# Performance work log

Measured on AMD Instinct MI355X. Metric: run time of the kernel, lower is better.

The kernel has to match this reference:

```python
import jax, jax.numpy as jnp
import numpy as np

D_MODEL = 1024
N_STATE = 64
BASEWIDTH = 3
BC_SCALE = (D_MODEL / BASEWIDTH) ** -0.5  # 'mup' mode width_mult**-0.5
RMS_EPS = 1.1920928955078125e-07  # torch.finfo(float32).eps (RMSNorm eps=None default)


def setup_inputs() -> dict:
    key = jax.random.key(0)
    k1, k2, k3, k4 = jax.random.split(key, 4)
    Bsz, L = 4, 2048
    u = jax.random.normal(k1, (Bsz, D_MODEL, L), dtype=jnp.float32)
    A = jax.random.uniform(k2, (N_STATE,), dtype=jnp.float32) * 0.1  # buffer: rand(N)*A_scale
    B = (jax.random.normal(k3, (N_STATE, D_MODEL), dtype=jnp.float32) + 0.1) * BC_SCALE
    C = (jax.random.normal(k4, (N_STATE, D_MODEL), dtype=jnp.float32) + 0.1) * BC_SCALE
    D = jnp.ones((D_MODEL,), dtype=jnp.float32)
    norm_w = jnp.ones((D_MODEL,), dtype=jnp.float32)
    return {"L": L, "u": u, "A": A, "B": B, "C": C, "D": D, "norm_w": norm_w}


def _ssm(u, A, B, C, D, norm_w):
    # u: [b, d, l]
    scale = BC_SCALE  # applied to Bu, Cu in 'mup' hyperparam mode
    Bu = jnp.einsum('nd,bdl->bnl', B, u) * scale  # [b, n, l]
    Cu = jnp.einsum('nd,bdl->bnl', C, u) * scale  # [b, n, l]
    b, d, l = u.shape
    # shifted_delta == 1 (delta path commented out in source), so
    # h_{t} = A * h_{t-1} + Bu[:, :, t] (outer) u[:, :, t]
    h0 = jnp.zeros((b, d, A.shape[0]), dtype=u.dtype)

    def step(h, xs):
        bu_t, cu_t, u_t = xs  # [b,n], [b,n], [b,d]
        h = h * A + u_t[:, :, None] * bu_t[:, None, :]  # [b, d, n]
        y_t = jnp.einsum('bn,bdn->bd', cu_t, h)
        return h, y_t

    xs = (jnp.moveaxis(Bu, 2, 0), jnp.moveaxis(Cu, 2, 0), jnp.moveaxis(u, 2, 0))
    _, y = jax.lax.scan(step, h0, xs)  # y: [l, b, d]
    y = jnp.moveaxis(y, 0, 2).transpose(1, 0, 2) if False else jnp.transpose(y, (1, 2, 0))  # [b, d, l]
    out = y + u * D[None, :, None]
    # RMSNorm over d_model (apply in [b, l, d] layout)
    x = jnp.transpose(out, (0, 2, 1))  # [b, l, d]
    ms = jnp.mean(x * x, axis=-1, keepdims=True)
    x = x * jax.lax.rsqrt(ms + RMS_EPS) * norm_w
    return jnp.transpose(x, (0, 2, 1))  # [b, d, l]


def reference(L, u, A, B, C, D, norm_w):
    del L  # sequence length == u.shape[-1]
    return _ssm(u, A, B, C, D, norm_w)
```

## Files before the change

kernel.cpp:

```cpp
#include <hip/hip_runtime.h>
#include <stdint.h>

#define DM 1024
#define LS 2048
#define RMS_EPS 1.1920928955078125e-07f
#define S2 0.0029296875f

typedef __attribute__((ext_vector_type(8))) short bf16x8;
typedef __attribute__((ext_vector_type(4))) float f32x4;
typedef __attribute__((ext_vector_type(2))) unsigned int u32x2;

__device__ __forceinline__ unsigned short f2bf(float f) {
  uint32_t u = __builtin_bit_cast(uint32_t, f);
  u += 0x7FFFu + ((u >> 16) & 1u);
  return (unsigned short)(u >> 16);
}

__global__ __launch_bounds__(256) void k0_prep(const float* __restrict__ B,
                                               const float* __restrict__ C,
                                               unsigned short* __restrict__ Bbf) {
  int i4 = blockIdx.x * 256 + threadIdx.x;
  const float4* src = (i4 < 16384) ? (const float4*)B : (const float4*)C;
  float4 v = src[i4 & 16383];
  ushort4 o;
  o.x = f2bf(v.x); o.y = f2bf(v.y); o.z = f2bf(v.z); o.w = f2bf(v.w);
  ((ushort4*)Bbf)[i4] = o;
}

__global__ __launch_bounds__(256) void kg(const float* __restrict__ u,
                                          const unsigned short* __restrict__ Bbf,
                                          const float* __restrict__ A,
                                          float* __restrict__ Kwg) {
  const int wg = blockIdx.x;
  const int sw = (wg & 7) * 64 + (wg >> 3);
  const int b  = sw >> 7;
  const int t0 = (sw & 127) * 16;
  const int tid  = threadIdx.x;
  const int lane = tid & 63;
  const int w    = tid >> 6;
  const int nn = lane & 15, q = lane >> 4;
  const float* ub = u + (size_t)b * DM * LS;

  __shared__ __align__(16) bf16x8 At[2][128][9];
  __shared__ __align__(16) bf16x8 Ut[2][8][33];
  __shared__ float KwS[16][20];
  float (*BuCu)[132] = (float (*)[132])&At[0][0][0];

  bf16x8 areg[4];
  float4 ureg[4];
  const int ukq = tid >> 3;
  const int ulq = tid & 7;
  const int ugc = t0 - 16 + 4*ulq;

  auto LOAD = [&](int kk) {
    #pragma unroll
    for (int h = 0; h < 4; ++h) {
      int id = tid + 256*h;
      areg[h] = *(const bf16x8*)(Bbf + (size_t)(id >> 3) * DM + 64*kk + 8*(id & 7));
    }
    if (tid < 128) {
      if (ugc >= 0) {
        #pragma unroll
        for (int r = 0; r < 4; ++r)
          ureg[r] = *(const float4*)(ub + (size_t)(64*kk + 4*ukq + r) * LS + ugc);
      } else {
        #pragma unroll
        for (int r = 0; r < 4; ++r) ureg[r] = make_float4(0.f, 0.f, 0.f, 0.f);
      }
    }
  };
  auto WRITE = [&](int buf) {
    #pragma unroll
    for (int h = 0; h < 4; ++h) {
      int id = tid + 256*h;
      At[buf][id >> 3][id & 7] = areg[h];
    }
    if (tid < 128) {
      #pragma unroll
      for (int i = 0; i < 4; ++i) {
        u32x2 pk;
        pk[0] = (unsigned)f2bf(((const float*)&ureg[0])[i]) |
                ((unsigned)f2bf(((const float*)&ureg[1])[i]) << 16);
        pk[1] = (unsigned)f2bf(((const float*)&ureg[2])[i]) |
                ((unsigned)f2bf(((const float*)&ureg[3])[i]) << 16);
        char* dst = (char*)&Ut[buf][ukq >> 1][4*ulq + i] + (ukq & 1) * 8;
        *(u32x2*)dst = pk;
      }
    }
  };

  f32x4 acc[2][2] = {};
  auto COMPUTE = [&](int buf) {
    #pragma unroll
    for (int kc = 0; kc < 2; ++kc) {
      bf16x8 bf0 = Ut[buf][4*kc + q][nn];
      bf16x8 bf1 = Ut[buf][4*kc + q][16 + nn];
      #pragma unroll
      for (int rt = 0; rt < 2; ++rt) {
        bf16x8 af = At[buf][32*w + 16*rt + nn][4*kc + q];
        acc[rt][0] = __builtin_amdgcn_mfma_f32_16x16x32_bf16(af, bf0, acc[rt][0], 0, 0, 0);
        acc[rt][1] = __builtin_amdgcn_mfma_f32_16x16x32_bf16(af, bf1, acc[rt][1], 0, 0, 0);
      }
    }
  };

  LOAD(0); WRITE(0); __syncthreads();
  for (int kk = 0; kk < 16; ++kk) {
    if (kk < 15) LOAD(kk + 1);
    COMPUTE(kk & 1);
    __syncthreads();
    if (kk < 15) { WRITE((kk + 1) & 1); __syncthreads(); }
  }

  #pragma unroll
  for (int rt = 0; rt < 2; ++rt)
    #pragma unroll
    for (int cn = 0; cn < 2; ++cn)
      *(f32x4*)&BuCu[16*cn + nn][32*w + 16*rt + 4*q] = acc[rt][cn];
  __syncthreads();

  {
    const int t = tid >> 4, p = tid & 15;
    const float4 cu = *(const float4*)&BuCu[16 + t][64 + 4*p];
    const float4 aa = *(const float4*)(A + 4*p);
    float pw0 = cu.x * S2, pw1 = cu.y * S2, pw2 = cu.z * S2, pw3 = cu.w * S2;
    #pragma unroll
    for (int j = 0; j < 16; ++j) {
      const float4 b4 = *(const float4*)&BuCu[16 + t - j][4*p];
      float s = pw0*b4.x + pw1*b4.y + pw2*b4.z + pw3*b4.w;
      s += __shfl_xor(s, 1, 64);
      s += __shfl_xor(s, 2, 64);
      s += __shfl_xor(s, 4, 64);
      s += __shfl_xor(s, 8, 64);
      if (p == 0) KwS[t][j] = s;
      pw0 *= aa.x; pw1 *= aa.y; pw2 *= aa.z; pw3 *= aa.w;
    }
  }
  __syncthreads();
  if (tid < 64) {
    const int t = tid >> 2, jq = tid & 3;
    *(float4*)(Kwg + ((size_t)b * LS + t0 + t) * 16 + 4*jq) =
        *(const float4*)&KwS[t][4*jq];
  }
}

__global__ __launch_bounds__(512) void kc(const float* __restrict__ u,
                                          const float* __restrict__ Kwg,
                                          const float* __restrict__ Dv,
                                          const float* __restrict__ nw,
                                          float* __restrict__ out) {
  const int wg = blockIdx.x;
  const int sw = (wg & 7) * 64 + (wg >> 3);
  const int b  = sw >> 7;
  const int t0 = (sw & 127) * 16;
  const int tid  = threadIdx.x;
  const int lane = tid & 63;
  const int w    = tid >> 6;
  const float* ub = u + (size_t)b * DM * LS;
  float* ob = out + (size_t)b * DM * LS;

  __shared__ float KwS[16][20];
  __shared__ float SSr[8][16];
  __shared__ float rsqv[16];

  if (tid < 64) {
    const int t = tid >> 2, jq = tid & 3;
    *(float4*)&KwS[t][4*jq] =
        *(const float4*)(Kwg + ((size_t)b * LS + t0 + t) * 16 + 4*jq);
  }
  __syncthreads();

  const int tg = tid & 3;
  const int dr = tid >> 2;
  const int cbase = t0 - 16 + 4*tg;
  float y[8][4];
  float ps[4] = {0.f, 0.f, 0.f, 0.f};
  #pragma unroll 1
  for (int c = 0; c < 8; ++c) {
    const int d = dr + 128*c;
    const float* rowp = ub + (size_t)d * LS;
    float wr[20];
    #pragma unroll
    for (int s5 = 0; s5 < 5; ++s5) {
      int g = cbase + 4*s5;
      float4 v = (g >= 0) ? *(const float4*)(rowp + g)
                          : make_float4(0.f, 0.f, 0.f, 0.f);
      wr[4*s5+0] = v.x; wr[4*s5+1] = v.y; wr[4*s5+2] = v.z; wr[4*s5+3] = v.w;
    }
    const float Dd = Dv[d];
    #pragma unroll
    for (int k = 0; k < 4; ++k) {
      f32x4 kv0 = *(const f32x4*)&KwS[4*tg + k][0];
      f32x4 kv1 = *(const f32x4*)&KwS[4*tg + k][4];
      f32x4 kv2 = *(const f32x4*)&KwS[4*tg + k][8];
      f32x4 kv3 = *(const f32x4*)&KwS[4*tg + k][12];
      float acc = wr[16 + k] * Dd;
      #pragma unroll
      for (int j = 0; j < 4; ++j)  acc = fmaf(kv0[j], wr[16 + k - j],      acc);
      #pragma unroll
      for (int j = 0; j < 4; ++j)  acc = fmaf(kv1[j], wr[16 + k - (j+4)],  acc);
      #pragma unroll
      for (int j = 0; j < 4; ++j)  acc = fmaf(kv2[j], wr[16 + k - (j+8)],  acc);
      #pragma unroll
      for (int j = 0; j < 4; ++j)  acc = fmaf(kv3[j], wr[16 + k - (j+12)], acc);
      y[c][k] = acc;
      ps[k] = fmaf(acc, acc, ps[k]);
    }
  }

  #pragma unroll
  for (int k = 0; k < 4; ++k) {
    ps[k] += __shfl_xor(ps[k], 4, 64);
    ps[k] += __shfl_xor(ps[k], 8, 64);
    ps[k] += __shfl_xor(ps[k], 16, 64);
    ps[k] += __shfl_xor(ps[k], 32, 64);
  }
  if (lane < 4)
    *(float4*)&SSr[w][4*lane] = make_float4(ps[0], ps[1], ps[2], ps[3]);
  __syncthreads();
  if (tid < 16) {
    float s = 0.f;
    #pragma unroll
    for (int ww = 0; ww < 8; ++ww) s += SSr[ww][tid];
    rsqv[tid] = rsqrtf(s * (1.f/1024.f) + RMS_EPS);
  }
  __syncthreads();

  float rq[4];
  #pragma unroll
  for (int k = 0; k < 4; ++k) rq[k] = rsqv[4*tg + k];
  #pragma unroll 1
  for (int c = 0; c < 8; ++c) {
    const int d = dr + 128*c;
    const float wn2 = nw[d];
    float4 o;
    o.x = y[c][0] * rq[0] * wn2;
    o.y = y[c][1] * rq[1] * wn2;
    o.z = y[c][2] * rq[2] * wn2;
    o.w = y[c][3] * rq[3] * wn2;
    *(float4*)(ob + (size_t)d * LS + t0 + 4*tg) = o;
  }
}

extern "C" void kernel_launch(void* const* d_in, const int* in_sizes, int n_in,
                              void* d_out, int out_size, void* d_ws, size_t ws_size,
                              hipStream_t stream) {
  const float* u  = (const float*)d_in[1];
  const float* A  = (const float*)d_in[2];
  const float* B  = (const float*)d_in[3];
  const float* C  = (const float*)d_in[4];
  const float* Dv = (const float*)d_in[5];
  const float* nw = (const float*)d_in[6];
  float* out = (float*)d_out;

  float* Kwg = (float*)d_ws;
  unsigned short* Bbf = (unsigned short*)((char*)d_ws + (512u << 10));

  k0_prep<<<dim3(128), dim3(256), 0, stream>>>(B, C, Bbf);
  kg     <<<dim3(512), dim3(256), 0, stream>>>(u, Bbf, A, Kwg);
  kc     <<<dim3(512), dim3(512), 0, stream>>>(u, Kwg, Dv, nw, out);
}
```

Before: 138.2 us.

## Stage full u tile in LDS once; stream B/C fragments directly from global

```diff
diff --git a/kernel.cpp b/kernel.cpp
--- a/kernel.cpp
+++ b/kernel.cpp
@@ -8,7 +8,6 @@
 
 typedef __attribute__((ext_vector_type(8))) short bf16x8;
 typedef __attribute__((ext_vector_type(4))) float f32x4;
-typedef __attribute__((ext_vector_type(2))) unsigned int u32x2;
 
 __device__ __forceinline__ unsigned short f2bf(float f) {
   uint32_t u = __builtin_bit_cast(uint32_t, f);
@@ -41,76 +40,55 @@
   const int nn = lane & 15, q = lane >> 4;
   const float* ub = u + (size_t)b * DM * LS;
 
-  __shared__ __align__(16) bf16x8 At[2][128][9];
-  __shared__ __align__(16) bf16x8 Ut[2][8][33];
+  __shared__ __align__(16) bf16x8 tile[128][32];
   __shared__ float KwS[16][20];
-  float (*BuCu)[132] = (float (*)[132])&At[0][0][0];
-
-  bf16x8 areg[4];
-  float4 ureg[4];
-  const int ukq = tid >> 3;
-  const int ulq = tid & 7;
-  const int ugc = t0 - 16 + 4*ulq;
-
-  auto LOAD = [&](int kk) {
-    #pragma unroll
-    for (int h = 0; h < 4; ++h) {
-      int id = tid + 256*h;
-      areg[h] = *(const bf16x8*)(Bbf + (size_t)(id >> 3) * DM + 64*kk + 8*(id & 7));
-    }
-    if (tid < 128) {
-      if (ugc >= 0) {
+  float (*BuCu)[132] = (float (*)[132])&tile[0][0];
+
+  {
+    const int kq = lane >> 3;
+    const int lo = lane & 7;
+    const int gcol = t0 - 16 + 4*lo;
+    #pragma unroll
+    for (int hh = 0; hh < 4; ++hh) {
+      const int krow = 256*w + 32*kq + 8*hh;
+      float4 vv[8];
+      if (gcol >= 0) {
         #pragma unroll
-        for (int r = 0; r < 4; ++r)
-          ureg[r] = *(const float4*)(ub + (size_t)(64*kk + 4*ukq + r) * LS + ugc);
+        for (int r = 0; r < 8; ++r)
+          vv[r] = *(const float4*)(ub + (size_t)(krow + r) * LS + gcol);
       } else {
         #pragma unroll
-        for (int r = 0; r < 4; ++r) ureg[r] = make_float4(0.f, 0.f, 0.f, 0.f);
+        for (int r = 0; r < 8; ++r) vv[r] = make_float4(0.f, 0.f, 0.f, 0.f);
       }
-    }
-  };
-  auto WRITE = [&](int buf) {
-    #pragma unroll
-    for (int h = 0; h < 4; ++h) {
-      int id = tid + 256*h;
-      At[buf][id >> 3][id & 7] = areg[h];
-    }
-    if (tid < 128) {
-      #pragma unroll
-      for (int i = 0; i < 4; ++i) {
-        u32x2 pk;
-        pk[0] = (unsigned)f2bf(((const float*)&ureg[0])[i]) |
-                ((unsigned)f2bf(((const float*)&ureg[1])[i]) << 16);
-        pk[1] = (unsigned)f2bf(((const float*)&ureg[2])[i]) |
-                ((unsigned)f2bf(((const float*)&ureg[3])[i]) << 16);
-        char* dst = (char*)&Ut[buf][ukq >> 1][4*ulq + i] + (ukq & 1) * 8;
-        *(u32x2*)dst = pk;
+      const int k8 = krow >> 3;
+      #pragma unroll
+      for (int c = 0; c < 4; ++c) {
+        union { bf16x8 v; unsigned short s[8]; } t8;
+        #pragma unroll
+        for (int r = 0; r < 8; ++r) t8.s[r] = f2bf(((const float*)&vv[r])[c]);
+        tile[k8][(4*lo + c) ^ kq] = t8.v;
       }
     }
-  };
+  }
+  __syncthreads();
 
   f32x4 acc[2][2] = {};
-  auto COMPUTE = [&](int buf) {
-    #pragma unroll
-    for (int kc = 0; kc < 2; ++kc) {
-      bf16x8 bf0 = Ut[buf][4*kc + q][nn];
-      bf16x8 bf1 = Ut[buf][4*kc + q][16 + nn];
-      #pragma unroll
-      for (int rt = 0; rt < 2; ++rt) {
-        bf16x8 af = At[buf][32*w + 16*rt + nn][4*kc + q];
-        acc[rt][0] = __builtin_amdgcn_mfma_f32_16x16x32_bf16(af, bf0, acc[rt][0], 0, 0, 0);
-        acc[rt][1] = __builtin_amdgcn_mfma_f32_16x16x32_bf16(af, bf1, acc[rt][1], 0, 0, 0);
-      }
-    }
-  };
-
-  LOAD(0); WRITE(0); __syncthreads();
-  for (int kk = 0; kk < 16; ++kk) {
-    if (kk < 15) LOAD(kk + 1);
-    COMPUTE(kk & 1);
-    __syncthreads();
-    if (kk < 15) { WRITE((kk + 1) & 1); __syncthreads(); }
-  }
+  const unsigned short* arow0 = Bbf + (size_t)(32*w + nn) * DM + 8*q;
+  #pragma unroll 4
+  for (int it = 0; it < 32; ++it) {
+    const int sx = nn ^ (it & 7);
+    bf16x8 bf1 = tile[4*it + q][16 + sx];
+    bf16x8 af0 = *(const bf16x8*)(arow0 + 32*it);
+    bf16x8 af1 = *(const bf16x8*)(arow0 + (size_t)16*DM + 32*it);
+    acc[0][1] = __builtin_amdgcn_mfma_f32_16x16x32_bf16(af0, bf1, acc[0][1], 0, 0, 0);
+    acc[1][1] = __builtin_amdgcn_mfma_f32_16x16x32_bf16(af1, bf1, acc[1][1], 0, 0, 0);
+    if (w < 2) {
+      bf16x8 bf0 = tile[4*it + q][sx];
+      acc[0][0] = __builtin_amdgcn_mfma_f32_16x16x32_bf16(af0, bf0, acc[0][0], 0, 0, 0);
+      acc[1][0] = __builtin_amdgcn_mfma_f32_16x16x32_bf16(af1, bf0, acc[1][0], 0, 0, 0);
+    }
+  }
+  __syncthreads();
 
   #pragma unroll
   for (int rt = 0; rt < 2; ++rt)
```

After: 145.1 us. 1.05x slower.
